# Kernel optimization log

Hardware: AMD Instinct MI355X
Metric: run time of the kernel (lower is better)

The kernel has to match this reference:

```python
import jax, jax.numpy as jnp
import numpy as np

D = 512; NH = 8; NL = 6; DFF = 2048
TOK = 1024; APP = 3; V = TOK + APP; PAD = V - 1
B = 256; SENC = 16; LTGT = 62


def setup_inputs() -> dict:
    key = jax.random.key(0)
    ks = jax.random.split(key, 14)
    g = lambda k, shp, s=0.02: jax.random.normal(k, shp, jnp.float32) * s
    return dict(
        encoder_out=jax.random.normal(ks[0], (B, SENC, D), jnp.float32),
        point_out=jax.random.normal(ks[1], (B, D), jnp.float32),
        emb=g(ks[2], (V, D)),
        pos_embed=g(ks[3], (1, LTGT, D)),
        sa_inw=g(ks[4], (NL, 3 * D, D)), sa_inb=jnp.zeros((NL, 3 * D), jnp.float32),
        sa_outw=g(ks[5], (NL, D, D)), sa_outb=jnp.zeros((NL, D), jnp.float32),
        ca_inw=g(ks[6], (NL, 3 * D, D)), ca_inb=jnp.zeros((NL, 3 * D), jnp.float32),
        ca_outw=g(ks[7], (NL, D, D)), ca_outb=jnp.zeros((NL, D), jnp.float32),
        ln1_s=jnp.ones((NL, D), jnp.float32), ln1_b=jnp.zeros((NL, D), jnp.float32),
        ln2_s=jnp.ones((NL, D), jnp.float32), ln2_b=jnp.zeros((NL, D), jnp.float32),
        ln3_s=jnp.ones((NL, D), jnp.float32), ln3_b=jnp.zeros((NL, D), jnp.float32),
        ff1_w=g(ks[8], (NL, DFF, D)), ff1_b=jnp.zeros((NL, DFF), jnp.float32),
        ff2_w=g(ks[9], (NL, D, DFF)), ff2_b=jnp.zeros((NL, D), jnp.float32),
        out_w=g(ks[10], (V, D)), out_b=jnp.zeros((V,), jnp.float32),
        tgt=jax.random.randint(ks[11], (B, LTGT), 0, TOK),
    )


def _ln(x, s, b, eps=1e-5):
    m = x.mean(-1, keepdims=True)
    v = ((x - m) ** 2).mean(-1, keepdims=True)
    return (x - m) / jnp.sqrt(v + eps) * s + b


def _mha(q_in, kv_in, inw, inb, outw, outb, mask):
    # PyTorch MultiheadAttention with packed in_proj [3D, D]
    hd = D // NH
    wq, wk, wv = inw[:D], inw[D:2 * D], inw[2 * D:]
    bq, bk, bv = inb[:D], inb[D:2 * D], inb[2 * D:]
    Bq, Tq = q_in.shape[0], q_in.shape[1]
    Tk = kv_in.shape[1]
    q = (q_in @ wq.T + bq).reshape(Bq, Tq, NH, hd)
    k = (kv_in @ wk.T + bk).reshape(Bq, Tk, NH, hd)
    v = (kv_in @ wv.T + bv).reshape(Bq, Tk, NH, hd)
    s = jnp.einsum('bqhd,bkhd->bhqk', q, k) / np.float32(np.sqrt(hd))
    if mask is not None:
        s = s + mask
    a = jax.nn.softmax(s, axis=-1)
    o = jnp.einsum('bhqk,bkhd->bqhd', a, v).reshape(Bq, Tq, D)
    return o @ outw.T + outb


def reference(encoder_out, point_out, emb, pos_embed,
              sa_inw, sa_inb, sa_outw, sa_outb,
              ca_inw, ca_inb, ca_outw, ca_outb,
              ln1_s, ln1_b, ln2_s, ln2_b, ln3_s, ln3_b,
              ff1_w, ff1_b, ff2_w, ff2_b, out_w, out_b, tgt):
    # scheduled_sampling_ratio == 1.0 => the per-step loop always writes the
    # ground-truth token, so output_sequence == tgt[:, :-1] and the returned
    # tensor equals one full causal decoder pass over tgt[:, :-1].
    tokens = tgt[:, :-1]                      # [B, L], L = 61
    L = tokens.shape[1]
    neg = jnp.float32(-jnp.inf)
    causal = jnp.where(jnp.triu(jnp.ones((L, L), bool), 1), neg, 0.0)
    padm = jnp.where(tokens == PAD, neg, 0.0)[:, None, None, :]  # [B,1,1,L]
    mask = causal[None, None] + padm          # [B,1,L,L]
    mem = encoder_out[:, :1, :]               # memory length 1 (encoder_out[:, [0]])
    x = emb[tokens] + point_out[:, None, :] + pos_embed[0, :L]
    for i in range(NL):
        x = _ln(x + _mha(x, x, sa_inw[i], sa_inb[i], sa_outw[i], sa_outb[i], mask), ln1_s[i], ln1_b[i])
        x = _ln(x + _mha(x, mem, ca_inw[i], ca_inb[i], ca_outw[i], ca_outb[i], None), ln2_s[i], ln2_b[i])
        h = jax.nn.relu(x @ ff1_w[i].T + ff1_b[i]) @ ff2_w[i].T + ff2_b[i]
        x = _ln(x + h, ln3_s[i], ln3_b[i])
    return x @ out_w.T + out_b               # [B, L, V]
```

## Files before the change

### kernel.cpp

```cpp
#include <hip/hip_runtime.h>
#include <stdint.h>
#include <stddef.h>

typedef unsigned short u16;
typedef float f4 __attribute__((ext_vector_type(4)));
typedef float f32x4 __attribute__((ext_vector_type(4)));
typedef short bf16x8 __attribute__((ext_vector_type(8)));
typedef u16 u16x4 __attribute__((ext_vector_type(4)));
typedef int i4v __attribute__((ext_vector_type(4)));

#define PAD_TOK 1026
#define LQ 61
#define NBATCH 256
#define MTOT (NBATCH * LQ)

__device__ __forceinline__ u16 f2b(float f) {
  uint32_t x = __float_as_uint(f);
  x += 0x7fff + ((x >> 16) & 1);
  return (u16)(x >> 16);
}
__device__ __forceinline__ float b2f(u16 u) {
  return __uint_as_float(((uint32_t)u) << 16);
}
__device__ __forceinline__ u16x4 cvt4(f4 v) {
  return (u16x4){f2b(v[0]), f2b(v[1]), f2b(v[2]), f2b(v[3])};
}

#define GLDS(gptr, lptr) __builtin_amdgcn_global_load_lds( \
    (const __attribute__((address_space(1))) void*)(gptr), \
    (__attribute__((address_space(3))) void*)(lptr), 16, 0, 0)

__device__ __forceinline__ bf16x8 ldfrag(const u16* buf, int row, int ksl, int kg) {
  const int chunk = (ksl * 4 + kg) ^ (row & 7);
  return *(const bf16x8*)&buf[row * 64 + chunk * 8];
}

__global__ __launch_bounds__(512) void gemm_bt3(
    const u16* __restrict__ A, const u16* __restrict__ W,
    const float* __restrict__ bias,
    float* __restrict__ Cf, u16* __restrict__ Cb,
    int N, int K, int Nreal, int ldc, int relu)
{
  __shared__ u16 SH[320 * 64];
  u16* const As = SH;
  u16* const Bs = SH + 4096;

  const int gx = gridDim.x;
  const int nwg = gx * gridDim.y;
  const int orig = blockIdx.y * gx + blockIdx.x;
  const int q8 = nwg >> 3, r8 = nwg & 7;
  const int xcd = orig & 7, off = orig >> 3;
  const int nid = (xcd < r8 ? xcd * (q8 + 1) : r8 * (q8 + 1) + (xcd - r8) * q8) + off;
  const int bx = nid % gx, by = nid / gx;

  const int tid = threadIdx.x;
  const int wid = tid >> 6, lane = tid & 63;
  const int wm = wid >> 2, wn = wid & 3;
  const long m0 = (long)by * 64;
  const long n0 = (long)bx * 256;

  const int lr = lane >> 3;
  const int lc = lane & 7;
  const int scol = ((lc ^ lr) << 3);

  f32x4 acc[2][4];
#pragma unroll
  for (int i = 0; i < 2; ++i)
#pragma unroll
    for (int j = 0; j < 4; ++j) acc[i][j] = (f32x4){0.f, 0.f, 0.f, 0.f};

  const u16* Abase = A + m0 * K;
  const u16* Wbase = W + n0 * K;
  const int r = lane & 15, kg = lane >> 4;

  for (int kt = 0; kt < K; kt += 64) {
    {
      const int arow = wid * 8;
      GLDS(Abase + (long)(arow + lr) * K + kt + scol, &As[arow * 64]);
#pragma unroll
      for (int c = 0; c < 4; ++c) {
        const int row = wid * 32 + c * 8;
        GLDS(Wbase + (long)(row + lr) * K + kt + scol, &Bs[row * 64]);
      }
    }
    __syncthreads();

#pragma unroll
    for (int ks = 0; ks < 2; ++ks) {
      bf16x8 a0 = ldfrag(As, wm * 32 + r, ks, kg);
      bf16x8 a1 = ldfrag(As, wm * 32 + 16 + r, ks, kg);
#pragma unroll
      for (int ni = 0; ni < 4; ++ni) {
        bf16x8 b = ldfrag(Bs, wn * 64 + ni * 16 + r, ks, kg);
        acc[0][ni] = __builtin_amdgcn_mfma_f32_16x16x32_bf16(a0, b, acc[0][ni], 0, 0, 0);
        acc[1][ni] = __builtin_amdgcn_mfma_f32_16x16x32_bf16(a1, b, acc[1][ni], 0, 0, 0);
      }
    }
    __syncthreads();
  }

  const int cr4 = (lane >> 4) * 4;
  const int cc = lane & 15;

  if (Cb) {
#pragma unroll
    for (int ni = 0; ni < 4; ++ni) {
      const int coll = wn * 64 + ni * 16 + cc;
      const float bv = bias[(int)n0 + coll];
#pragma unroll
      for (int mi = 0; mi < 2; ++mi) {
#pragma unroll
        for (int j = 0; j < 4; ++j) {
          const int rowl = wm * 32 + mi * 16 + cr4 + j;
          float v = acc[mi][ni][j] + bv;
          if (relu) v = fmaxf(v, 0.f);
          const int phys = (coll >> 3) ^ (rowl & 31);
          SH[rowl * 256 + phys * 8 + (coll & 7)] = f2b(v);
        }
      }
    }
    __syncthreads();
#pragma unroll
    for (int i = 0; i < 4; ++i) {
      const int t = i * 512 + tid;
      const int row = t >> 5, ch = t & 31;
      const int n = (int)n0 + ch * 8;
      const int phys = ch ^ (row & 31);
      *(bf16x8*)&Cb[(m0 + row) * (long)N + n] =
          *(const bf16x8*)&SH[row * 256 + phys * 8];
    }
  } else {
    float* SHf = (float*)SH;
#pragma unroll
    for (int p = 0; p < 2; ++p) {
      if (wm == p) {
#pragma unroll
        for (int ni = 0; ni < 4; ++ni) {
          const int coll = wn * 64 + ni * 16 + cc;
          const float bv = bias[(int)n0 + coll];
#pragma unroll
          for (int mi = 0; mi < 2; ++mi) {
#pragma unroll
            for (int j = 0; j < 4; ++j) {
              const int rowl = mi * 16 + cr4 + j;
              float v = acc[mi][ni][j] + bv;
              if (relu) v = fmaxf(v, 0.f);
              SHf[rowl * 260 + coll] = v;
            }
          }
        }
      }
      __syncthreads();
      {
        const int row = tid >> 4, c = tid & 15;
        const int nbase = (int)n0 + c * 16;
        const long gro = (m0 + p * 32 + row) * (long)ldc;
        if (nbase + 16 <= Nreal) {
#pragma unroll
          for (int e = 0; e < 16; ++e)
            Cf[gro + nbase + e] = SHf[row * 260 + c * 16 + e];
        } else if (nbase < Nreal) {
          for (int e = 0; e < Nreal - nbase; ++e)
            Cf[gro + nbase + e] = SHf[row * 260 + c * 16 + e];
        }
      }
      __syncthreads();
    }
  }
}

template<int BM>
__global__ __launch_bounds__(256) void gemm_bt(
    const u16* __restrict__ A, const u16* __restrict__ W,
    const float* __restrict__ bias,
    float* __restrict__ Cf, u16* __restrict__ Cb,
    int M, int N, int K, int Nreal, int ldc, int relu,
    long aZ, long wZ, long bZ, long cZ)
{
  constexpr int MI = BM / 32;
  const int z = blockIdx.z;
  A += z * aZ; W += z * wZ; bias += z * bZ;
  if (Cf) Cf += z * cZ;
  if (Cb) Cb += z * cZ;

  __shared__ u16 As[BM * 64];
  __shared__ u16 Bs[128 * 64];

  const int gx = gridDim.x;
  const int nwg = gx * gridDim.y;
  const int orig = blockIdx.y * gx + blockIdx.x;
  const int q8 = nwg >> 3, r8 = nwg & 7;
  const int xcd = orig & 7, off = orig >> 3;
  const int nid = (xcd < r8 ? xcd * (q8 + 1) : r8 * (q8 + 1) + (xcd - r8) * q8) + off;
  const int bx = nid % gx, by = nid / gx;

  const int tid = threadIdx.x;
  const int wid = tid >> 6, lane = tid & 63;
  const int wr = wid >> 1, wc = wid & 1;
  const long m0 = (long)by * BM;
  const long n0 = (long)bx * 128;

  const int lr = lane >> 3;
  const int lc = lane & 7;
  const int scol = ((lc ^ lr) << 3);

  f32x4 acc[MI][4];
#pragma unroll
  for (int i = 0; i < MI; ++i)
#pragma unroll
    for (int j = 0; j < 4; ++j) acc[i][j] = (f32x4){0.f, 0.f, 0.f, 0.f};

  const u16* Abase = A + m0 * K;
  const u16* Wbase = W + n0 * K;
  const int r = lane & 15, kg = lane >> 4;

  for (int kt = 0; kt < K; kt += 64) {
#pragma unroll
    for (int c = 0; c < BM / 32; ++c) {
      const int row = wid * (BM / 4) + c * 8;
      GLDS(Abase + (long)(row + lr) * K + kt + scol, &As[row * 64]);
    }
#pragma unroll
    for (int c = 0; c < 4; ++c) {
      const int row = wid * 32 + c * 8;
      GLDS(Wbase + (long)(row + lr) * K + kt + scol, &Bs[row * 64]);
    }
    __syncthreads();

#pragma unroll
    for (int ks = 0; ks < 2; ++ks) {
      bf16x8 a[MI], b[4];
#pragma unroll
      for (int mi = 0; mi < MI; ++mi)
        a[mi] = ldfrag(As, wr * (BM / 2) + mi * 16 + r, ks, kg);
#pragma unroll
      for (int ni = 0; ni < 4; ++ni)
        b[ni] = ldfrag(Bs, wc * 64 + ni * 16 + r, ks, kg);
#pragma unroll
      for (int mi = 0; mi < MI; ++mi)
#pragma unroll
        for (int ni = 0; ni < 4; ++ni)
          acc[mi][ni] = __builtin_amdgcn_mfma_f32_16x16x32_bf16(a[mi], b[ni], acc[mi][ni], 0, 0, 0);
    }
    __syncthreads();
  }

  const int cr4 = (lane >> 4) * 4;
  const int cc = lane & 15;

  if (Cb) {
#pragma unroll
    for (int ni = 0; ni < 4; ++ni) {
      const int coll = wc * 64 + ni * 16 + cc;
      const float bv = bias[(int)n0 + coll];
#pragma unroll
      for (int mi = 0; mi < MI; ++mi) {
#pragma unroll
        for (int j = 0; j < 4; ++j) {
          const int rowl = wr * (BM / 2) + mi * 16 + cr4 + j;
          float v = acc[mi][ni][j] + bv;
          if (relu) v = fmaxf(v, 0.f);
          const int sw = (rowl & 7) << 3;
          u16* half = (coll & 64) ? Bs : As;
          half[rowl * 64 + ((coll & 63) ^ sw)] = f2b(v);
        }
      }
    }
    __syncthreads();
    constexpr int PT = BM / 16;
#pragma unroll
    for (int i = 0; i < PT; ++i) {
      const int t = i * 256 + tid;
      const int row = t >> 4, ch = t & 15;
      const int n = (int)n0 + ch * 8;
      if (n < Nreal) {
        const int phys = (ch & 7) ^ (row & 7);
        const u16* half = (ch < 8) ? As : Bs;
        bf16x8 vv = *(const bf16x8*)&half[row * 64 + phys * 8];
        *(bf16x8*)&Cb[(m0 + row) * (long)N + n] = vv;
      }
    }
  } else {
#pragma unroll
    for (int ni = 0; ni < 4; ++ni) {
      const int n = (int)n0 + wc * 64 + ni * 16 + cc;
      if (n >= Nreal) continue;
      const float bv = bias[n];
#pragma unroll
      for (int mi = 0; mi < MI; ++mi) {
#pragma unroll
        for (int j = 0; j < 4; ++j) {
          const long m = m0 + wr * (BM / 2) + mi * 16 + cr4 + j;
          float v = acc[mi][ni][j] + bv;
          if (relu) v = fmaxf(v, 0.f);
          Cf[m * ldc + n] = v;
        }
      }
    }
  }
}

__global__ __launch_bounds__(512) void gemmln_k(
    const u16* __restrict__ A, const u16* __restrict__ W,
    const float* __restrict__ bias,
    const u16* __restrict__ cavb,
    const float* __restrict__ s1w, const float* __restrict__ b1w,
    const float* __restrict__ s2w, const float* __restrict__ b2w,
    u16* __restrict__ XB, int K)
{
  __shared__ u16 LDSBUF[2][36864];
  __shared__ float LSTAT[64][8];
  __shared__ u16 LCAV[1536];
  u16* const EP = &LDSBUF[0][0];

  const int nwg = gridDim.x;
  const int orig = blockIdx.x;
  const int q8 = nwg >> 3, r8 = nwg & 7;
  const int xcd = orig & 7, off = orig >> 3;
  const int by = (xcd < r8 ? xcd * (q8 + 1) : r8 * (q8 + 1) + (xcd - r8) * q8) + off;

  const int tid = threadIdx.x;
  const int wid = tid >> 6, lane = tid & 63;
  const int wm = wid >> 2, wn = wid & 3;
  const long m0 = (long)by * 64;

  const int lr = lane >> 3, lc = lane & 7;
  const int scol = ((lc ^ lr) << 3);
  const int r = lane & 15, kg = lane >> 4;

  f32x4 acc[2][8];
#pragma unroll
  for (int i = 0; i < 2; ++i)
#pragma unroll
    for (int j = 0; j < 8; ++j) acc[i][j] = (f32x4){0.f, 0.f, 0.f, 0.f};

  const u16* Abase = A + m0 * K;

#define STAGE(buf, kt) do {                                              \
    const int arow_ = wid * 8;                                           \
    GLDS(Abase + (long)(arow_ + lr) * K + (kt) + scol,                   \
         &(buf)[32768 + arow_ * 64]);                                    \
    _Pragma("unroll")                                                    \
    for (int c_ = 0; c_ < 8; ++c_) {                                     \
      const int row_ = wid * 64 + c_ * 8;                                \
      GLDS(W + (long)(row_ + lr) * K + (kt) + scol, &(buf)[row_ * 64]);  \
    }                                                                    \
  } while (0)

  const int nt = K >> 6;
  STAGE(LDSBUF[0], 0);
  asm volatile("s_waitcnt vmcnt(0)" ::: "memory");
  __builtin_amdgcn_sched_barrier(0);
  __builtin_amdgcn_s_barrier();

  for (int t = 0; t < nt; ++t) {
    u16* const bufc = &LDSBUF[t & 1][0];
    if (t + 1 < nt) STAGE(LDSBUF[(t + 1) & 1], (t + 1) << 6);
#pragma unroll
    for (int ks = 0; ks < 2; ++ks) {
      bf16x8 a0 = ldfrag(bufc + 32768, wm * 32 + r, ks, kg);
      bf16x8 a1 = ldfrag(bufc + 32768, wm * 32 + 16 + r, ks, kg);
      __builtin_amdgcn_s_setprio(1);
#pragma unroll
      for (int ni = 0; ni < 8; ++ni) {
        bf16x8 b = ldfrag(bufc, wn * 128 + ni * 16 + r, ks, kg);
        acc[0][ni] = __builtin_amdgcn_mfma_f32_16x16x32_bf16(a0, b, acc[0][ni], 0, 0, 0);
        acc[1][ni] = __builtin_amdgcn_mfma_f32_16x16x32_bf16(a1, b, acc[1][ni], 0, 0, 0);
      }
      __builtin_amdgcn_s_setprio(0);
    }
    asm volatile("s_waitcnt vmcnt(0)" ::: "memory");
    __builtin_amdgcn_sched_barrier(0);
    __builtin_amdgcn_s_barrier();
  }
#undef STAGE

  const int b0 = (int)(m0 / LQ);
  const int bsplit1 = (b0 + 1) * LQ;
  const int bsplit2 = (b0 + 2) * LQ;

#pragma unroll
  for (int i = 0; i < 8; ++i) {
    const int t = i * 512 + tid;
    const int row = t >> 6, ch = t & 63;
    *(bf16x8*)&EP[row * 516 + ch * 8] =
        *(const bf16x8*)&XB[(m0 + row) * 512 + ch * 8];
  }
  for (int t = tid; t < 1536; t += 512) {
    const int bb = t >> 9, c = t & 511;
    int bi = b0 + bb;
    if (bi > NBATCH - 1) bi = NBATCH - 1;
    LCAV[bb * 512 + c] = cavb[(long)bi * 512 + c];
  }
  __syncthreads();

  float bcol[8];
#pragma unroll
  for (int ni = 0; ni < 8; ++ni) bcol[ni] = bias[wn * 128 + ni * 16 + r];
#pragma unroll
  for (int mi = 0; mi < 2; ++mi)
#pragma unroll
    for (int ni = 0; ni < 8; ++ni) {
      const int col = wn * 128 + ni * 16 + r;
#pragma unroll
      for (int j = 0; j < 4; ++j) {
        const int row = wm * 32 + mi * 16 + kg * 4 + j;
        acc[mi][ni][j] += bcol[ni] + b2f(EP[row * 516 + col]);
      }
    }

#pragma unroll
  for (int mi = 0; mi < 2; ++mi)
#pragma unroll
    for (int j = 0; j < 4; ++j) {
      float s1 = 0.f, s2 = 0.f;
#pragma unroll
      for (int ni = 0; ni < 8; ++ni) {
        const float v = acc[mi][ni][j];
        s1 += v; s2 += v * v;
      }
#pragma unroll
      for (int o = 1; o < 16; o <<= 1) {
        s1 += __shfl_xor(s1, o);
        s2 += __shfl_xor(s2, o);
      }
      if (r == 0) {
        const int row = wm * 32 + mi * 16 + kg * 4 + j;
        LSTAT[row][wn] = s1;
        LSTAT[row][4 + wn] = s2;
      }
    }
  __syncthreads();

  float sc[8], bc[8];
#pragma unroll
  for (int ni = 0; ni < 8; ++ni) {
    const int col = wn * 128 + ni * 16 + r;
    sc[ni] = s1w[col]; bc[ni] = b1w[col];
  }
#pragma unroll
  for (int mi = 0; mi < 2; ++mi)
#pragma unroll
    for (int j = 0; j < 4; ++j) {
      const int row = wm * 32 + mi * 16 + kg * 4 + j;
      const float S1 = LSTAT[row][0] + LSTAT[row][1] + LSTAT[row][2] + LSTAT[row][3];
      const float S2 = LSTAT[row][4] + LSTAT[row][5] + LSTAT[row][6] + LSTAT[row][7];
      const float mean = S1 * (1.f / 512.f);
      const float var = S2 * (1.f / 512.f) - mean * mean;
      const float rstd = rsqrtf(var + 1e-5f);
#pragma unroll
      for (int ni = 0; ni < 8; ++ni)
        acc[mi][ni][j] = (acc[mi][ni][j] - mean) * rstd * sc[ni] + bc[ni];
    }

#pragma unroll
  for (int mi = 0; mi < 2; ++mi)
#pragma unroll
    for (int j = 0; j < 4; ++j) {
      const int row = wm * 32 + mi * 16 + kg * 4 + j;
      const int gr = (int)m0 + row;
      const int sel = (gr >= bsplit2) ? 2 : ((gr >= bsplit1) ? 1 : 0);
#pragma unroll
      for (int ni = 0; ni < 8; ++ni) {
        const int col = wn * 128 + ni * 16 + r;
        acc[mi][ni][j] += b2f(LCAV[sel * 512 + col]);
      }
    }
  __syncthreads();
#pragma unroll
  for (int mi = 0; mi < 2; ++mi)
#pragma unroll
    for (int j = 0; j < 4; ++j) {
      float s1 = 0.f, s2 = 0.f;
#pragma unroll
      for (int ni = 0; ni < 8; ++ni) {
        const float v = acc[mi][ni][j];
        s1 += v; s2 += v * v;
      }
#pragma unroll
      for (int o = 1; o < 16; o <<= 1) {
        s1 += __shfl_xor(s1, o);
        s2 += __shfl_xor(s2, o);
      }
      if (r == 0) {
        const int row = wm * 32 + mi * 16 + kg * 4 + j;
        LSTAT[row][wn] = s1;
        LSTAT[row][4 + wn] = s2;
      }
    }
  __syncthreads();
#pragma unroll
  for (int ni = 0; ni < 8; ++ni) {
    const int col = wn * 128 + ni * 16 + r;
    sc[ni] = s2w[col]; bc[ni] = b2w[col];
  }
#pragma unroll
  for (int mi = 0; mi < 2; ++mi)
#pragma unroll
    for (int j = 0; j < 4; ++j) {
      const int row = wm * 32 + mi * 16 + kg * 4 + j;
      const float S1 = LSTAT[row][0] + LSTAT[row][1] + LSTAT[row][2] + LSTAT[row][3];
      const float S2 = LSTAT[row][4] + LSTAT[row][5] + LSTAT[row][6] + LSTAT[row][7];
      const float mean = S1 * (1.f / 512.f);
      const float var = S2 * (1.f / 512.f) - mean * mean;
      const float rstd = rsqrtf(var + 1e-5f);
#pragma unroll
      for (int ni = 0; ni < 8; ++ni)
        acc[mi][ni][j] = (acc[mi][ni][j] - mean) * rstd * sc[ni] + bc[ni];
    }

#pragma unroll
  for (int mi = 0; mi < 2; ++mi)
#pragma unroll
    for (int ni = 0; ni < 8; ++ni) {
      const int col = wn * 128 + ni * 16 + r;
#pragma unroll
      for (int j = 0; j < 4; ++j) {
        const int row = wm * 32 + mi * 16 + kg * 4 + j;
        EP[row * 516 + col] = f2b(acc[mi][ni][j]);
      }
    }
  __syncthreads();
#pragma unroll
  for (int i = 0; i < 8; ++i) {
    const int t = i * 512 + tid;
    const int row = t >> 6, ch = t & 63;
    *(bf16x8*)&XB[(m0 + row) * 512 + ch * 8] =
        *(const bf16x8*)&EP[row * 516 + ch * 8];
  }
}

__global__ __launch_bounds__(256) void attn_k(const u16* __restrict__ qkv,
                                              const int* __restrict__ tgt,
                                              u16* __restrict__ outp)
{
  __shared__ u16 Qs[64 * 72];
  __shared__ u16 Ks[64 * 72];
  __shared__ u16 Vt[64 * 72];
  __shared__ float S[64 * 65];
  __shared__ int stok[64];

  const int bid = blockIdx.x;
  const int b = bid >> 3, h = bid & 7;
  const int tid = threadIdx.x;
  const int tr = tid >> 2, seg = tid & 3;

  if (tid < 64) stok[tid] = (tid < 61) ? tgt[b * 62 + tid] : -1;

  const long rowbase = ((long)(b * LQ + tr)) * 1536 + h * 64;
  if (tr < LQ) {
    const i4v* qsrc = (const i4v*)(qkv + rowbase + seg * 16);
    i4v q0 = qsrc[0], q1 = qsrc[1];
    *(i4v*)&Qs[tr * 72 + seg * 16] = q0;
    *(i4v*)&Qs[tr * 72 + seg * 16 + 8] = q1;
    const i4v* ksrc = (const i4v*)(qkv + rowbase + 512 + seg * 16);
    i4v k0 = ksrc[0], k1 = ksrc[1];
    *(i4v*)&Ks[tr * 72 + seg * 16] = k0;
    *(i4v*)&Ks[tr * 72 + seg * 16 + 8] = k1;
    const u16* vsrc = qkv + rowbase + 1024 + seg * 16;
#pragma unroll
    for (int i = 0; i < 16; ++i) Vt[(seg * 16 + i) * 72 + tr] = vsrc[i];
  } else {
    i4v zz = {0, 0, 0, 0};
    *(i4v*)&Qs[tr * 72 + seg * 16] = zz;
    *(i4v*)&Qs[tr * 72 + seg * 16 + 8] = zz;
    *(i4v*)&Ks[tr * 72 + seg * 16] = zz;
    *(i4v*)&Ks[tr * 72 + seg * 16 + 8] = zz;
#pragma unroll
    for (int i = 0; i < 16; ++i) Vt[(seg * 16 + i) * 72 + tr] = 0;
  }
  __syncthreads();

  const int lane = tid & 63, w = tid >> 6;
  const int r = lane & 15, kg = lane >> 4;

  {
    f32x4 s[4];
#pragma unroll
    for (int ni = 0; ni < 4; ++ni) s[ni] = (f32x4){0.f, 0.f, 0.f, 0.f};
    bf16x8 a0 = *(const bf16x8*)&Qs[(w * 16 + r) * 72 + kg * 8];
    bf16x8 a1 = *(const bf16x8*)&Qs[(w * 16 + r) * 72 + 32 + kg * 8];
#pragma unroll
    for (int ni = 0; ni < 4; ++ni) {
      bf16x8 b0 = *(const bf16x8*)&Ks[(ni * 16 + r) * 72 + kg * 8];
      bf16x8 b1 = *(const bf16x8*)&Ks[(ni * 16 + r) * 72 + 32 + kg * 8];
      s[ni] = __builtin_amdgcn_mfma_f32_16x16x32_bf16(a0, b0, s[ni], 0, 0, 0);
      s[ni] = __builtin_amdgcn_mfma_f32_16x16x32_bf16(a1, b1, s[ni], 0, 0, 0);
    }
#pragma unroll
    for (int ni = 0; ni < 4; ++ni)
#pragma unroll
      for (int j = 0; j < 4; ++j)
        S[(w * 16 + kg * 4 + j) * 65 + ni * 16 + r] = s[ni][j];
  }
  __syncthreads();

  {
    const int row = tid >> 2, g = tid & 3;
    float vals[16];
    float mx = -3e38f;
#pragma unroll
    for (int i = 0; i < 16; ++i) {
      const int k = g * 16 + i;
      float v = S[row * 65 + k] * 0.125f;
      const bool ok = (k <= row) && (k < LQ) && (stok[k] != PAD_TOK);
      v = ok ? v : -1e30f;
      vals[i] = v;
      mx = fmaxf(mx, v);
    }
    mx = fmaxf(mx, __shfl_xor(mx, 1));
    mx = fmaxf(mx, __shfl_xor(mx, 2));
    float sum = 0.f;
#pragma unroll
    for (int i = 0; i < 16; ++i) { float e = __expf(vals[i] - mx); vals[i] = e; sum += e; }
    sum += __shfl_xor(sum, 1);
    sum += __shfl_xor(sum, 2);
    const float inv = 1.f / sum;
#pragma unroll
    for (int i = 0; i < 16; ++i) Qs[row * 72 + g * 16 + i] = f2b(vals[i] * inv);
  }
  __syncthreads();

  {
    f32x4 o[4];
#pragma unroll
    for (int ni = 0; ni < 4; ++ni) o[ni] = (f32x4){0.f, 0.f, 0.f, 0.f};
    bf16x8 a0 = *(const bf16x8*)&Qs[(w * 16 + r) * 72 + kg * 8];
    bf16x8 a1 = *(const bf16x8*)&Qs[(w * 16 + r) * 72 + 32 + kg * 8];
#pragma unroll
    for (int ni = 0; ni < 4; ++ni) {
      bf16x8 b0 = *(const bf16x8*)&Vt[(ni * 16 + r) * 72 + kg * 8];
      bf16x8 b1 = *(const bf16x8*)&Vt[(ni * 16 + r) * 72 + 32 + kg * 8];
      o[ni] = __builtin_amdgcn_mfma_f32_16x16x32_bf16(a0, b0, o[ni], 0, 0, 0);
      o[ni] = __builtin_amdgcn_mfma_f32_16x16x32_bf16(a1, b1, o[ni], 0, 0, 0);
    }
#pragma unroll
    for (int ni = 0; ni < 4; ++ni)
#pragma unroll
      for (int j = 0; j < 4; ++j) {
        const int qrow = w * 16 + kg * 4 + j;
        const int col = ni * 16 + r;
        Ks[qrow * 64 + (col ^ ((qrow & 7) << 3))] = f2b(o[ni][j]);
      }
  }
  __syncthreads();

  {
    const int row = tid >> 2, sub = tid & 3;
    if (row < LQ) {
      const long obase = ((long)(b * LQ + row)) * 512 + h * 64;
#pragma unroll
      for (int i = 0; i < 2; ++i) {
        const int ch = i * 4 + sub;
        const int phys = ch ^ (row & 7);
        bf16x8 vv = *(const bf16x8*)&Ks[row * 64 + phys * 8];
        *(bf16x8*)&outp[obase + ch * 8] = vv;
      }
    }
  }
}

__device__ __forceinline__ void ln_row(f4& v0, f4& v1,
                                       const float* __restrict__ sw,
                                       const float* __restrict__ bw, int d0) {
  float s1 = v0[0] + v0[1] + v0[2] + v0[3] + v1[0] + v1[1] + v1[2] + v1[3];
  float s2 = v0[0]*v0[0] + v0[1]*v0[1] + v0[2]*v0[2] + v0[3]*v0[3]
           + v1[0]*v1[0] + v1[1]*v1[1] + v1[2]*v1[2] + v1[3]*v1[3];
#pragma unroll
  for (int off = 1; off < 64; off <<= 1) {
    s1 += __shfl_xor(s1, off);
    s2 += __shfl_xor(s2, off);
  }
  const float mean = s1 * (1.f / 512.f);
  const float var = s2 * (1.f / 512.f) - mean * mean;
  const float rstd = rsqrtf(var + 1e-5f);
  const f4* sp = (const f4*)(sw + d0);
  const f4* bp = (const f4*)(bw + d0);
  f4 ss0 = sp[0], ss1 = sp[1], bb0 = bp[0], bb1 = bp[1];
#pragma unroll
  for (int i = 0; i < 4; ++i) {
    v0[i] = (v0[i] - mean) * rstd * ss0[i] + bb0[i];
    v1[i] = (v1[i] - mean) * rstd * ss1[i] + bb1[i];
  }
}

__global__ __launch_bounds__(256) void lnf3_k(const u16* __restrict__ p,
                                              const u16* __restrict__ xr,
                                              const float* __restrict__ s1,
                                              const float* __restrict__ b1,
                                              u16* __restrict__ out)
{
  const int m = blockIdx.x * 4 + (threadIdx.x >> 6);
  const int lane = threadIdx.x & 63;
  const int d0 = lane * 8;
  bf16x8 pv = *(const bf16x8*)(p + (long)m * 512 + d0);
  bf16x8 xv = *(const bf16x8*)(xr + (long)m * 512 + d0);
  f4 v0, v1;
#pragma unroll
  for (int i = 0; i < 4; ++i) {
    v0[i] = b2f((u16)pv[i]) + b2f((u16)xv[i]);
    v1[i] = b2f((u16)pv[4 + i]) + b2f((u16)xv[4 + i]);
  }
  ln_row(v0, v1, s1, b1, d0);
  u16x4* ob = (u16x4*)(out + (long)m * 512 + d0);
  ob[0] = cvt4(v0);
  ob[1] = cvt4(v1);
}

__global__ __launch_bounds__(256) void embed_k(const float* __restrict__ emb,
                                               const float* __restrict__ pout,
                                               const float* __restrict__ pos,
                                               const int* __restrict__ tgt,
                                               u16* __restrict__ XB)
{
  const int m = blockIdx.x * 4 + (threadIdx.x >> 6);
  const int lane = threadIdx.x & 63;
  const int b = m / LQ, t = m % LQ;
  const int tok = tgt[b * 62 + t];
  const int d0 = lane * 8;
  const f4* e = (const f4*)(emb + (long)tok * 512 + d0);
  const f4* p = (const f4*)(pout + (long)b * 512 + d0);
  const f4* q = (const f4*)(pos + (long)t * 512 + d0);
  f4 v0 = e[0] + p[0] + q[0];
  f4 v1 = e[1] + p[1] + q[1];
  u16x4* xb = (u16x4*)(XB + (long)m * 512 + d0);
  xb[0] = cvt4(v0);
  xb[1] = cvt4(v1);
}

__global__ void cvtall_k(const float* __restrict__ sa_inw, const float* __restrict__ sa_outw,
                         const float* __restrict__ ca_outw, const float* __restrict__ ff1_w,
                         const float* __restrict__ ff2_w, const float* __restrict__ ca_inw,
                         const float* __restrict__ out_w, const float* __restrict__ out_b,
                         const float* __restrict__ enc,
                         u16* __restrict__ WSA, u16* __restrict__ WSO,
                         u16* __restrict__ WCO, u16* __restrict__ WF1,
                         u16* __restrict__ WF2, u16* __restrict__ WCAV,
                         u16* __restrict__ WOUT, float* __restrict__ BOUT,
                         u16* __restrict__ MEMB)
{
  const int C0 = 320;
  const int C1 = C0 + 32768;
  const int C2 = C1 + 163840;
  const int C3 = C2 + 393216;
  const int C4 = C3 + 1179648;
  const int C5 = C4 + 393216;
  const int C6 = C5 + 393216;
  const int C7 = C6 + 1572864;
  const int C8 = C7 + 1572864;
  for (int i = blockIdx.x * 256 + threadIdx.x; i < C8; i += gridDim.x * 256) {
    if (i < C0) {
      const int base = i * 4;
#pragma unroll
      for (int e = 0; e < 4; ++e)
        BOUT[base + e] = (base + e < 1027) ? out_b[base + e] : 0.f;
    } else if (i < C1) {
      const int k = i - C0;
      const int b = (k * 4) >> 9, d = (k * 4) & 511;
      f4 v = ((const f4*)enc)[(b * 8192 + d) >> 2];
      ((u16x4*)MEMB)[k] = cvt4(v);
    } else if (i < C2) {
      const int k = i - C1;
      const int row = (k * 4) >> 9;
      u16x4 o = {0, 0, 0, 0};
      if (row < 1027) { f4 v = ((const f4*)out_w)[k]; o = cvt4(v); }
      ((u16x4*)WOUT)[k] = o;
    } else if (i < C3) {
      const int k = i - C2;
      const int l = k >> 16, rem = k & 65535;
      f4 v = ((const f4*)ca_inw)[l * 196608 + 131072 + rem];
      ((u16x4*)WCAV)[k] = cvt4(v);
    } else {
      const float* s; u16* d; int k;
      if (i < C4)      { s = sa_inw;  d = WSA; k = i - C3; }
      else if (i < C5) { s = sa_outw; d = WSO; k = i - C4; }
      else if (i < C6) { s = ca_outw; d = WCO; k = i - C5; }
      else if (i < C7) { s = ff1_w;   d = WF1; k = i - C6; }
      else             { s = ff2_w;   d = WF2; k = i - C7; }
      f4 v = ((const f4*)s)[k];
      ((u16x4*)d)[k] = cvt4(v);
    }
  }
}

static constexpr size_t XB_OFF    = 0;
static constexpr size_t P_OFF     = 15990784;
static constexpr size_t BIG_OFF   = 31981568;
static constexpr size_t ATT_OFF   = 95944704;
static constexpr size_t WSA_OFF   = 111935488;
static constexpr size_t WSO_OFF   = 121372672;
static constexpr size_t WCAV_OFF  = 124518400;
static constexpr size_t WCO_OFF   = 127664128;
static constexpr size_t WF1_OFF   = 130809856;
static constexpr size_t WF2_OFF   = 143392768;
static constexpr size_t WOUT_OFF  = 155975680;
static constexpr size_t BOUT_OFF  = 157286400;
static constexpr size_t MEMB_OFF  = 157291520;
static constexpr size_t CATMP_OFF = 157553664;
static constexpr size_t CAVB_OFF  = 159126528;

extern "C" void kernel_launch(void* const* d_in, const int* in_sizes, int n_in,
                              void* d_out, int out_size, void* d_ws, size_t ws_size,
                              hipStream_t stream) {
  (void)in_sizes; (void)n_in; (void)out_size; (void)ws_size;
  const float* encoder_out = (const float*)d_in[0];
  const float* point_out   = (const float*)d_in[1];
  const float* emb         = (const float*)d_in[2];
  const float* pos         = (const float*)d_in[3];
  const float* sa_inw      = (const float*)d_in[4];
  const float* sa_inb      = (const float*)d_in[5];
  const float* sa_outw     = (const float*)d_in[6];
  const float* sa_outb     = (const float*)d_in[7];
  const float* ca_inw      = (const float*)d_in[8];
  const float* ca_inb      = (const float*)d_in[9];
  const float* ca_outw     = (const float*)d_in[10];
  const float* ca_outb     = (const float*)d_in[11];
  const float* ln1_s       = (const float*)d_in[12];
  const float* ln1_b       = (const float*)d_in[13];
  const float* ln2_s       = (const float*)d_in[14];
  const float* ln2_b       = (const float*)d_in[15];
  const float* ln3_s       = (const float*)d_in[16];
  const float* ln3_b       = (const float*)d_in[17];
  const float* ff1_w       = (const float*)d_in[18];
  const float* ff1_b       = (const float*)d_in[19];
  const float* ff2_w       = (const float*)d_in[20];
  const float* ff2_b       = (const float*)d_in[21];
  const float* out_w       = (const float*)d_in[22];
  const float* out_b       = (const float*)d_in[23];
  const int*   tgt         = (const int*)d_in[24];

  char* ws = (char*)d_ws;
  u16*   XB    = (u16*)(ws + XB_OFF);
  u16*   P     = (u16*)(ws + P_OFF);
  u16*   BIG   = (u16*)(ws + BIG_OFF);
  u16*   ATT   = (u16*)(ws + ATT_OFF);
  u16*   WSA   = (u16*)(ws + WSA_OFF);
  u16*   WSO   = (u16*)(ws + WSO_OFF);
  u16*   WCAV  = (u16*)(ws + WCAV_OFF);
  u16*   WCO   = (u16*)(ws + WCO_OFF);
  u16*   WF1   = (u16*)(ws + WF1_OFF);
  u16*   WF2   = (u16*)(ws + WF2_OFF);
  u16*   WOUT  = (u16*)(ws + WOUT_OFF);
  float* BOUT  = (float*)(ws + BOUT_OFF);
  u16*   MEMB  = (u16*)(ws + MEMB_OFF);
  u16*   CATMP = (u16*)(ws + CATMP_OFF);
  u16*   CAVB  = (u16*)(ws + CAVB_OFF);

  cvtall_k<<<dim3(2048), dim3(256), 0, stream>>>(
      sa_inw, sa_outw, ca_outw, ff1_w, ff2_w, ca_inw, out_w, out_b, encoder_out,
      WSA, WSO, WCO, WF1, WF2, WCAV, WOUT, BOUT, MEMB);

  embed_k<<<dim3(MTOT / 4), dim3(256), 0, stream>>>(emb, point_out, pos, tgt, XB);

  gemm_bt<64><<<dim3(4, 4, 6), dim3(256), 0, stream>>>(
      MEMB, WCAV, ca_inb + 1024, nullptr, CATMP,
      256, 512, 512, 512, 512, 0,
      0L, 262144L, 1536L, 131072L);
  gemm_bt<64><<<dim3(4, 4, 6), dim3(256), 0, stream>>>(
      CATMP, WCO, ca_outb, nullptr, CAVB,
      256, 512, 512, 512, 512, 0,
      131072L, 262144L, 512L, 131072L);

  for (int l = 0; l < 6; ++l) {
    gemm_bt3<<<dim3(6, 244), dim3(512), 0, stream>>>(
        XB, WSA + (long)l * 786432, sa_inb + l * 1536, nullptr, BIG,
        1536, 512, 1536, 1536, 0);
    attn_k<<<dim3(2048), dim3(256), 0, stream>>>(BIG, tgt, ATT);
    gemmln_k<<<dim3(244), dim3(512), 0, stream>>>(
        ATT, WSO + (long)l * 262144, sa_outb + l * 512,
        CAVB + (long)l * 131072,
        ln1_s + l * 512, ln1_b + l * 512, ln2_s + l * 512, ln2_b + l * 512,
        XB, 512);
    gemm_bt3<<<dim3(8, 244), dim3(512), 0, stream>>>(
        XB, WF1 + (long)l * 1048576, ff1_b + l * 2048, nullptr, BIG,
        2048, 512, 2048, 2048, 1);
    gemm_bt3<<<dim3(2, 244), dim3(512), 0, stream>>>(
        BIG, WF2 + (long)l * 1048576, ff2_b + l * 512, nullptr, P,
        512, 2048, 512, 512, 0);
    lnf3_k<<<dim3(MTOT / 4), dim3(256), 0, stream>>>(
        P, XB, ln3_s + l * 512, ln3_b + l * 512, XB);
  }

  gemm_bt3<<<dim3(5, 244), dim3(512), 0, stream>>>(
      XB, WOUT, BOUT, (float*)d_out, nullptr,
      1280, 512, 1027, 1027, 0);
}
```

Before: 1.113 ms.

## Add 64x512-tile FF1 GEMM with XCD remap, fold embedding into convert kernel

Adds a new GEMM kernel for the FF1 projection. It uses a 64x512 output tile per 512-thread block and remaps block IDs across the 8 XCDs, so the A tile is loaded once per 512 output columns and neighbouring blocks share L2. Results are staged through swizzled LDS for vectorised bf16 stores. The embedding kernel is folded into the weight-conversion kernel to save one launch. MFMA sections are also wrapped in s_setprio. The larger tile uses more accumulator registers and about 72KB of LDS, which may reduce occupancy.

```diff
diff --git a/kernel.cpp b/kernel.cpp
--- a/kernel.cpp
+++ b/kernel.cpp
@@ -89,12 +89,14 @@
     for (int ks = 0; ks < 2; ++ks) {
       bf16x8 a0 = ldfrag(As, wm * 32 + r, ks, kg);
       bf16x8 a1 = ldfrag(As, wm * 32 + 16 + r, ks, kg);
+      __builtin_amdgcn_s_setprio(1);
 #pragma unroll
       for (int ni = 0; ni < 4; ++ni) {
         bf16x8 b = ldfrag(Bs, wn * 64 + ni * 16 + r, ks, kg);
         acc[0][ni] = __builtin_amdgcn_mfma_f32_16x16x32_bf16(a0, b, acc[0][ni], 0, 0, 0);
         acc[1][ni] = __builtin_amdgcn_mfma_f32_16x16x32_bf16(a1, b, acc[1][ni], 0, 0, 0);
       }
+      __builtin_amdgcn_s_setprio(0);
     }
     __syncthreads();
   }
@@ -166,6 +168,99 @@
       }
       __syncthreads();
     }
+  }
+}
+
+__global__ __launch_bounds__(512) void gemm_bn512(
+    const u16* __restrict__ A, const u16* __restrict__ W,
+    const float* __restrict__ bias, u16* __restrict__ Cb,
+    int N, int K, int relu)
+{
+  __shared__ u16 SH[36864];
+  u16* const Bs = SH;
+  u16* const As = SH + 32768;
+
+  const int gx = gridDim.x;
+  const int nwg = gx * gridDim.y;
+  const int orig = blockIdx.y * gx + blockIdx.x;
+  const int q8 = nwg >> 3, r8 = nwg & 7;
+  const int xcd = orig & 7, off = orig >> 3;
+  const int nid = (xcd < r8 ? xcd * (q8 + 1) : r8 * (q8 + 1) + (xcd - r8) * q8) + off;
+  const int bx = nid % gx, by = nid / gx;
+
+  const int tid = threadIdx.x;
+  const int wid = tid >> 6, lane = tid & 63;
+  const int wm = wid >> 2, wn = wid & 3;
+  const long m0 = (long)by * 64;
+  const long n0 = (long)bx * 512;
+
+  const int lr = lane >> 3, lc = lane & 7;
+  const int scol = ((lc ^ lr) << 3);
+  const int r = lane & 15, kg = lane >> 4;
+
+  f32x4 acc[2][8];
+#pragma unroll
+  for (int i = 0; i < 2; ++i)
+#pragma unroll
+    for (int j = 0; j < 8; ++j) acc[i][j] = (f32x4){0.f, 0.f, 0.f, 0.f};
+
+  const u16* Abase = A + m0 * K;
+  const u16* Wbase = W + n0 * K;
+
+  for (int kt = 0; kt < K; kt += 64) {
+    {
+      const int arow = wid * 8;
+      GLDS(Abase + (long)(arow + lr) * K + kt + scol, &As[arow * 64]);
+#pragma unroll
+      for (int c = 0; c < 8; ++c) {
+        const int row = wid * 64 + c * 8;
+        GLDS(Wbase + (long)(row + lr) * K + kt + scol, &Bs[row * 64]);
+      }
+    }
+    __syncthreads();
+#pragma unroll
+    for (int ks = 0; ks < 2; ++ks) {
+      bf16x8 a0 = ldfrag(As, wm * 32 + r, ks, kg);
+      bf16x8 a1 = ldfrag(As, wm * 32 + 16 + r, ks, kg);
+      __builtin_amdgcn_s_setprio(1);
+#pragma unroll
+      for (int ni = 0; ni < 8; ++ni) {
+        bf16x8 b = ldfrag(Bs, wn * 128 + ni * 16 + r, ks, kg);
+        acc[0][ni] = __builtin_amdgcn_mfma_f32_16x16x32_bf16(a0, b, acc[0][ni], 0, 0, 0);
+        acc[1][ni] = __builtin_amdgcn_mfma_f32_16x16x32_bf16(a1, b, acc[1][ni], 0, 0, 0);
+      }
+      __builtin_amdgcn_s_setprio(0);
+    }
+    __syncthreads();
+  }
+
+  const int cr4 = (lane >> 4) * 4;
+  const int cc = lane & 15;
+#pragma unroll
+  for (int ni = 0; ni < 8; ++ni) {
+    const int coll = wn * 128 + ni * 16 + cc;
+    const float bv = bias[(int)n0 + coll];
+#pragma unroll
+    for (int mi = 0; mi < 2; ++mi) {
+#pragma unroll
+      for (int j = 0; j < 4; ++j) {
+        const int rowl = wm * 32 + mi * 16 + cr4 + j;
+        float v = acc[mi][ni][j] + bv;
+        if (relu) v = fmaxf(v, 0.f);
+        const int phys = (coll >> 3) ^ rowl;
+        SH[rowl * 512 + phys * 8 + (coll & 7)] = f2b(v);
+      }
+    }
+  }
+  __syncthreads();
+#pragma unroll
+  for (int i = 0; i < 8; ++i) {
+    const int t = i * 512 + tid;
+    const int row = t >> 6, ch = t & 63;
+    const int n = (int)n0 + ch * 8;
+    const int phys = ch ^ row;
+    *(bf16x8*)&Cb[(m0 + row) * (long)N + n] =
+        *(const bf16x8*)&SH[row * 512 + phys * 8];
   }
 }
 
@@ -707,37 +802,18 @@
   ob[1] = cvt4(v1);
 }
 
-__global__ __launch_bounds__(256) void embed_k(const float* __restrict__ emb,
-                                               const float* __restrict__ pout,
-                                               const float* __restrict__ pos,
-                                               const int* __restrict__ tgt,
-                                               u16* __restrict__ XB)
-{
-  const int m = blockIdx.x * 4 + (threadIdx.x >> 6);
-  const int lane = threadIdx.x & 63;
-  const int b = m / LQ, t = m % LQ;
-  const int tok = tgt[b * 62 + t];
-  const int d0 = lane * 8;
-  const f4* e = (const f4*)(emb + (long)tok * 512 + d0);
-  const f4* p = (const f4*)(pout + (long)b * 512 + d0);
-  const f4* q = (const f4*)(pos + (long)t * 512 + d0);
-  f4 v0 = e[0] + p[0] + q[0];
-  f4 v1 = e[1] + p[1] + q[1];
-  u16x4* xb = (u16x4*)(XB + (long)m * 512 + d0);
-  xb[0] = cvt4(v0);
-  xb[1] = cvt4(v1);
-}
-
 __global__ void cvtall_k(const float* __restrict__ sa_inw, const float* __restrict__ sa_outw,
                          const float* __restrict__ ca_outw, const float* __restrict__ ff1_w,
                          const float* __restrict__ ff2_w, const float* __restrict__ ca_inw,
                          const float* __restrict__ out_w, const float* __restrict__ out_b,
                          const float* __restrict__ enc,
+                         const float* __restrict__ emb, const float* __restrict__ pout,
+                         const float* __restrict__ pos, const int* __restrict__ tgt,
                          u16* __restrict__ WSA, u16* __restrict__ WSO,
                          u16* __restrict__ WCO, u16* __restrict__ WF1,
                          u16* __restrict__ WF2, u16* __restrict__ WCAV,
                          u16* __restrict__ WOUT, float* __restrict__ BOUT,
-                         u16* __restrict__ MEMB)
+                         u16* __restrict__ MEMB, u16* __restrict__ XB)
 {
   const int C0 = 320;
   const int C1 = C0 + 32768;
@@ -748,7 +824,8 @@
   const int C6 = C5 + 393216;
   const int C7 = C6 + 1572864;
   const int C8 = C7 + 1572864;
-  for (int i = blockIdx.x * 256 + threadIdx.x; i < C8; i += gridDim.x * 256) {
+  const int C9 = C8 + 1998848;
+  for (int i = blockIdx.x * 256 + threadIdx.x; i < C9; i += gridDim.x * 256) {
     if (i < C0) {
       const int base = i * 4;
 #pragma unroll
@@ -770,7 +847,7 @@
       const int l = k >> 16, rem = k & 65535;
       f4 v = ((const f4*)ca_inw)[l * 196608 + 131072 + rem];
       ((u16x4*)WCAV)[k] = cvt4(v);
-    } else {
+    } else if (i < C8) {
       const float* s; u16* d; int k;
       if (i < C4)      { s = sa_inw;  d = WSA; k = i - C3; }
       else if (i < C5) { s = sa_outw; d = WSO; k = i - C4; }
@@ -779,6 +856,15 @@
       else             { s = ff2_w;   d = WF2; k = i - C7; }
       f4 v = ((const f4*)s)[k];
       ((u16x4*)d)[k] = cvt4(v);
+    } else {
+      const int k = i - C8;
+      const int m = k >> 7, d4 = k & 127;
+      const int b = m / LQ, t = m - b * LQ;
+      const int tok = tgt[b * 62 + t];
+      f4 v = ((const f4*)emb)[tok * 128 + d4]
+           + ((const f4*)pout)[b * 128 + d4]
+           + ((const f4*)pos)[t * 128 + d4];
+      ((u16x4*)XB)[k] = cvt4(v);
     }
   }
 }
@@ -848,9 +934,8 @@
 
   cvtall_k<<<dim3(2048), dim3(256), 0, stream>>>(
       sa_inw, sa_outw, ca_outw, ff1_w, ff2_w, ca_inw, out_w, out_b, encoder_out,
-      WSA, WSO, WCO, WF1, WF2, WCAV, WOUT, BOUT, MEMB);
-
-  embed_k<<<dim3(MTOT / 4), dim3(256), 0, stream>>>(emb, point_out, pos, tgt, XB);
+      emb, point_out, pos, tgt,
+      WSA, WSO, WCO, WF1, WF2, WCAV, WOUT, BOUT, MEMB, XB);
 
   gemm_bt<64><<<dim3(4, 4, 6), dim3(256), 0, stream>>>(
       MEMB, WCAV, ca_inb + 1024, nullptr, CATMP,
@@ -871,9 +956,9 @@
         CAVB + (long)l * 131072,
         ln1_s + l * 512, ln1_b + l * 512, ln2_s + l * 512, ln2_b + l * 512,
         XB, 512);
-    gemm_bt3<<<dim3(8, 244), dim3(512), 0, stream>>>(
-        XB, WF1 + (long)l * 1048576, ff1_b + l * 2048, nullptr, BIG,
-        2048, 512, 2048, 2048, 1);
+    gemm_bn512<<<dim3(4, 244), dim3(512), 0, stream>>>(
+        XB, WF1 + (long)l * 1048576, ff1_b + l * 2048, BIG,
+        2048, 512, 1);
     gemm_bt3<<<dim3(2, 244), dim3(512), 0, stream>>>(
         BIG, WF2 + (long)l * 1048576, ff2_b + l * 512, nullptr, P,
         512, 2048, 512, 512, 0);
```

Result: no change. 1.121 ms (+0.7%).
